# Performance work log

Measured on AMD Instinct MI355X. Metric: run time of the kernel, lower is better.

The kernel has to match this reference:

```python
import jax, jax.numpy as jnp
import numpy as np

K_FRAC = 0.5
NUM_CLASSES = 16
N = 8192
IN_DIM = 512
PER_CLASS = N // NUM_CLASSES          # 512 items per class (equal counts -> static shapes)
KK = int(K_FRAC * PER_CLASS)          # 256 kept per class


def setup_inputs() -> dict:
    key = jax.random.key(0)
    k1, k2, k3, k4 = jax.random.split(key, 4)
    M = jax.random.normal(k1, (1, N, N), dtype=jnp.float32)
    X = jax.random.normal(k2, (1, N, IN_DIM), dtype=jnp.float32)
    # class ids with exactly PER_CLASS members per class, randomly permuted
    mask = jax.random.permutation(k3, jnp.arange(N, dtype=jnp.int64) % NUM_CLASSES)[None, :]
    W = jax.random.normal(k4, (1, IN_DIM), dtype=jnp.float32) * 0.02
    b = jnp.zeros((1,), dtype=jnp.float32)
    return {"M": M, "X": X, "mask": mask, "W": W, "b": b}


def reference(M, X, mask, W, b):
    # scores = sigmoid(Linear(X) / 100), squeezed to [N] (batch == 1)
    scores = jax.nn.sigmoid((jnp.einsum('bnd,od->bno', X, W)[0, :, 0] + b[0]) / 100.0)  # [N]
    m0 = mask[-1]  # [N] class ids
    idx_parts, val_parts = [], []
    for j in range(NUM_CLASSES):  # fixed small loop over classes
        idx_j = jnp.nonzero(m0 == j, size=PER_CLASS, fill_value=0)[0]   # [PER_CLASS]
        way_scores = scores[idx_j]
        # top-k smallest of (way_scores - mean) == top-k largest of (mean - way_scores)
        _, way_idx = jax.lax.top_k(jnp.mean(way_scores) - way_scores, KK)
        val_parts.append(way_scores[way_idx])
        idx_parts.append(idx_j[way_idx])
    values = jnp.concatenate(val_parts)          # [NUM_CLASSES*KK]
    idx = jnp.concatenate(idx_parts)             # [NUM_CLASSES*KK]
    X_out = X[:, idx, :] * values[None, :, None] # gather + scale
    M_out = M[:, idx, :][:, :, idx]              # double gather (rows then cols)
    return (M_out, X_out, mask[:, idx])
```

## Files before the change

### kernel.cpp

```cpp
#include <hip/hip_runtime.h>

#define NN 8192
#define IN_DIM 512
#define NUM_CLASSES 16
#define PER_CLASS 512
#define KK 256
#define NSEL (NUM_CLASSES * KK)

typedef float vfloat4 __attribute__((ext_vector_type(4)));

__global__ __launch_bounds__(256) void scores_kernel(
    const float* __restrict__ X, const float* __restrict__ W,
    const float* __restrict__ b, float* __restrict__ scores) {
  const int wave = threadIdx.x >> 6;
  const int lane = threadIdx.x & 63;
  const int row  = blockIdx.x * (blockDim.x >> 6) + wave;
  if (row >= NN) return;

  const float4* xp = (const float4*)(X + (size_t)row * IN_DIM);
  const float4* wp = (const float4*)W;
  float acc = 0.f;
#pragma unroll
  for (int k = 0; k < 2; ++k) {
    const int i = lane + k * 64;
    const float4 xv = xp[i];
    const float4 wv = wp[i];
    acc += xv.x * wv.x + xv.y * wv.y + xv.z * wv.z + xv.w * wv.w;
  }
#pragma unroll
  for (int off = 32; off > 0; off >>= 1)
    acc += __shfl_xor(acc, off, 64);

  if (lane == 0) {
    const float z = (acc + b[0]) * 0.01f;
    scores[row] = 1.0f / (1.0f + expf(-z));
  }
}

__global__ __launch_bounds__(512) void select_kernel(
    const int* __restrict__ mask, const float* __restrict__ scores,
    int* __restrict__ sel_idx, float* __restrict__ sel_val) {
  const int cls  = blockIdx.x;
  const int tid  = threadIdx.x;
  const int lane = tid & 63;
  const int wave = tid >> 6;

  __shared__ int   members[PER_CLASS];
  __shared__ float ssc[PER_CLASS];
  __shared__ int   wave_tot[8];
  __shared__ int   running;
  __shared__ double wsum[8];
  __shared__ float meanf;

  if (tid == 0) running = 0;
  __syncthreads();

  for (int chunk = 0; chunk < NN; chunk += 512) {
    const int i = chunk + tid;
    const bool flag = (mask[i] == cls);
    const unsigned long long bal = __ballot(flag);
    const int pre = __popcll(bal & ((1ull << lane) - 1ull));
    if (lane == 0) wave_tot[wave] = __popcll(bal);
    __syncthreads();
    int woff = 0;
    for (int w = 0; w < wave; ++w) woff += wave_tot[w];
    const int pos = running + woff + pre;
    if (flag) members[pos] = i;
    __syncthreads();
    if (tid == 0) {
      int tot = 0;
      for (int w = 0; w < 8; ++w) tot += wave_tot[w];
      running += tot;
    }
    __syncthreads();
  }

  ssc[tid] = scores[members[tid]];
  __syncthreads();
  double v = (double)ssc[tid];
#pragma unroll
  for (int off = 32; off > 0; off >>= 1)
    v += __shfl_xor(v, off, 64);
  if (lane == 0) wsum[wave] = v;
  __syncthreads();
  if (tid == 0) {
    double s = 0.0;
    for (int w = 0; w < 8; ++w) s += wsum[w];
    meanf = (float)(s / (double)PER_CLASS);
  }
  __syncthreads();

  const float m = meanf;
  const float mykey = m - ssc[tid];
  int rank = 0;
  for (int u = 0; u < PER_CLASS; ++u) {
    const float ku = m - ssc[u];
    rank += (ku > mykey) || (ku == mykey && u < tid);
  }
  if (rank < KK) {
    sel_val[cls * KK + rank] = ssc[tid];
    sel_idx[cls * KK + rank] = members[tid];
  }
}

__global__ __launch_bounds__(512) void gather_kernel(
    const float* __restrict__ M, const float* __restrict__ X,
    const int* __restrict__ sel_idx, const float* __restrict__ sel_val,
    float* __restrict__ m_out, float* __restrict__ x_out,
    float* __restrict__ mask_out) {
  __shared__ float row[NN];
  const int r   = blockIdx.x;
  const int src = sel_idx[r];

  const vfloat4* mp = (const vfloat4*)(M + (size_t)src * NN);
  vfloat4* rp = (vfloat4*)row;
#pragma unroll
  for (int k = 0; k < 4; ++k) {
    const int i = k * 512 + threadIdx.x;
    rp[i] = __builtin_nontemporal_load(&mp[i]);
  }

  if (threadIdx.x < 128) {
    const float v = sel_val[r];
    const vfloat4 x =
        ((const vfloat4*)(X + (size_t)src * IN_DIM))[threadIdx.x];
    const vfloat4 o = x * v;
    __builtin_nontemporal_store(
        o, (vfloat4*)(x_out + (size_t)r * IN_DIM) + threadIdx.x);
  }
  if (threadIdx.x == 0) mask_out[r] = (float)(r >> 8);

  __syncthreads();

  vfloat4* out = (vfloat4*)(m_out + (size_t)r * NSEL);
  const int4* idx4 = (const int4*)sel_idx;
#pragma unroll
  for (int k = 0; k < 2; ++k) {
    const int c4 = k * 512 + threadIdx.x;
    const int4 id = idx4[c4];
    vfloat4 o;
    o.x = row[id.x]; o.y = row[id.y]; o.z = row[id.z]; o.w = row[id.w];
    __builtin_nontemporal_store(o, &out[c4]);
  }
}

extern "C" void kernel_launch(void* const* d_in, const int* in_sizes, int n_in,
                              void* d_out, int out_size, void* d_ws, size_t ws_size,
                              hipStream_t stream) {
  const float* M    = (const float*)d_in[0];
  const float* X    = (const float*)d_in[1];
  const int*   mask = (const int*)  d_in[2];
  const float* W    = (const float*)d_in[3];
  const float* b    = (const float*)d_in[4];

  float* out = (float*)d_out;
  float* m_out    = out;
  float* x_out    = out + (size_t)NSEL * NSEL;
  float* mask_out = x_out + (size_t)NSEL * IN_DIM;

  float* scores  = (float*)d_ws;
  int*   sel_idx = (int*)((char*)d_ws + NN * sizeof(float));
  float* sel_val = (float*)((char*)d_ws + NN * sizeof(float)
                                        + NSEL * sizeof(int));

  scores_kernel<<<NN / 4, 256, 0, stream>>>(X, W, b, scores);

  select_kernel<<<NUM_CLASSES, 512, 0, stream>>>(mask, scores, sel_idx, sel_val);

  gather_kernel<<<NSEL, 512, 0, stream>>>(M, X, sel_idx, sel_val,
                                          m_out, x_out, mask_out);
}
```

Baseline: 387.3 us.

## Fuse score and class-compaction into one kernel and split ranking across blocks

Class-member compaction moves out of the serial 16-chunk loop in select_kernel into a single pass inside a fused prep kernel. There, each thread scans 16 mask entries and the block does a wave prefix scan, running alongside the score blocks. The rank computation is spread over 4 blocks per class, with each output index split across 4 threads reading float4 keys and combining via shuffles. The gather kernel also hoists its index loads ahead of the row load. The intent is to shorten the small serial select stage that sits ahead of the bandwidth-bound gather, at the cost of recomputing the class mean in every block and extra workspace for the members array.

```diff
diff --git a/kernel.cpp b/kernel.cpp
--- a/kernel.cpp
+++ b/kernel.cpp
@@ -9,75 +9,88 @@
 
 typedef float vfloat4 __attribute__((ext_vector_type(4)));
 
-__global__ __launch_bounds__(256) void scores_kernel(
+__global__ __launch_bounds__(512) void prep_kernel(
     const float* __restrict__ X, const float* __restrict__ W,
-    const float* __restrict__ b, float* __restrict__ scores) {
-  const int wave = threadIdx.x >> 6;
-  const int lane = threadIdx.x & 63;
-  const int row  = blockIdx.x * (blockDim.x >> 6) + wave;
-  if (row >= NN) return;
-
-  const float4* xp = (const float4*)(X + (size_t)row * IN_DIM);
-  const float4* wp = (const float4*)W;
-  float acc = 0.f;
-#pragma unroll
-  for (int k = 0; k < 2; ++k) {
-    const int i = lane + k * 64;
-    const float4 xv = xp[i];
-    const float4 wv = wp[i];
-    acc += xv.x * wv.x + xv.y * wv.y + xv.z * wv.z + xv.w * wv.w;
-  }
-#pragma unroll
-  for (int off = 32; off > 0; off >>= 1)
-    acc += __shfl_xor(acc, off, 64);
-
-  if (lane == 0) {
-    const float z = (acc + b[0]) * 0.01f;
-    scores[row] = 1.0f / (1.0f + expf(-z));
-  }
-}
-
-__global__ __launch_bounds__(512) void select_kernel(
-    const int* __restrict__ mask, const float* __restrict__ scores,
-    int* __restrict__ sel_idx, float* __restrict__ sel_val) {
-  const int cls  = blockIdx.x;
+    const float* __restrict__ b, const int* __restrict__ mask,
+    float* __restrict__ scores, int* __restrict__ members) {
   const int tid  = threadIdx.x;
   const int lane = tid & 63;
   const int wave = tid >> 6;
 
-  __shared__ int   members[PER_CLASS];
-  __shared__ float ssc[PER_CLASS];
-  __shared__ int   wave_tot[8];
-  __shared__ int   running;
+  if (blockIdx.x < NUM_CLASSES) {
+    const int cls = blockIdx.x;
+    __shared__ int wave_tot[8];
+    const int base_i = tid * 16;
+    const int4* mp = (const int4*)(mask + base_i);
+    int flags = 0;
+#pragma unroll
+    for (int k = 0; k < 4; ++k) {
+      const int4 mv = mp[k];
+      flags |= (mv.x == cls) << (k * 4 + 0);
+      flags |= (mv.y == cls) << (k * 4 + 1);
+      flags |= (mv.z == cls) << (k * 4 + 2);
+      flags |= (mv.w == cls) << (k * 4 + 3);
+    }
+    const int cnt = __popc(flags);
+    int scan = cnt;
+#pragma unroll
+    for (int off = 1; off < 64; off <<= 1) {
+      const int n = __shfl_up(scan, off, 64);
+      if (lane >= off) scan += n;
+    }
+    if (lane == 63) wave_tot[wave] = scan;
+    __syncthreads();
+    int wbase = 0;
+    for (int w = 0; w < wave; ++w) wbase += wave_tot[w];
+    int pos = wbase + scan - cnt;
+    int* out = members + cls * PER_CLASS;
+    int f = flags;
+    while (f) {
+      const int k = __ffs(f) - 1;
+      f &= f - 1;
+      out[pos++] = base_i + k;
+    }
+  } else {
+    const int row = (blockIdx.x - NUM_CLASSES) * 8 + wave;
+    const float4* xp = (const float4*)(X + (size_t)row * IN_DIM);
+    const float4* wp = (const float4*)W;
+    float acc = 0.f;
+#pragma unroll
+    for (int k = 0; k < 2; ++k) {
+      const int i = lane + k * 64;
+      const float4 xv = xp[i];
+      const float4 wv = wp[i];
+      acc += xv.x * wv.x + xv.y * wv.y + xv.z * wv.z + xv.w * wv.w;
+    }
+#pragma unroll
+    for (int off = 32; off > 0; off >>= 1)
+      acc += __shfl_xor(acc, off, 64);
+    if (lane == 0) {
+      const float z = (acc + b[0]) * 0.01f;
+      scores[row] = 1.0f / (1.0f + expf(-z));
+    }
+  }
+}
+
+__global__ __launch_bounds__(512) void select_kernel(
+    const int* __restrict__ members, const float* __restrict__ scores,
+    int* __restrict__ sel_idx, float* __restrict__ sel_val) {
+  const int cls  = blockIdx.x >> 2;
+  const int q    = blockIdx.x & 3;
+  const int tid  = threadIdx.x;
+  const int lane = tid & 63;
+  const int wave = tid >> 6;
+
+  __shared__ float  ssc[PER_CLASS];
+  __shared__ float  keys[PER_CLASS];
   __shared__ double wsum[8];
-  __shared__ float meanf;
-
-  if (tid == 0) running = 0;
-  __syncthreads();
-
-  for (int chunk = 0; chunk < NN; chunk += 512) {
-    const int i = chunk + tid;
-    const bool flag = (mask[i] == cls);
-    const unsigned long long bal = __ballot(flag);
-    const int pre = __popcll(bal & ((1ull << lane) - 1ull));
-    if (lane == 0) wave_tot[wave] = __popcll(bal);
-    __syncthreads();
-    int woff = 0;
-    for (int w = 0; w < wave; ++w) woff += wave_tot[w];
-    const int pos = running + woff + pre;
-    if (flag) members[pos] = i;
-    __syncthreads();
-    if (tid == 0) {
-      int tot = 0;
-      for (int w = 0; w < 8; ++w) tot += wave_tot[w];
-      running += tot;
-    }
-    __syncthreads();
-  }
-
-  ssc[tid] = scores[members[tid]];
-  __syncthreads();
-  double v = (double)ssc[tid];
+  __shared__ float  meanf;
+
+  const int   mem_t = members[cls * PER_CLASS + tid];
+  const float sc_t  = scores[mem_t];
+  ssc[tid] = sc_t;
+
+  double v = (double)sc_t;
 #pragma unroll
   for (int off = 32; off > 0; off >>= 1)
     v += __shfl_xor(v, off, 64);
@@ -89,17 +102,30 @@
     meanf = (float)(s / (double)PER_CLASS);
   }
   __syncthreads();
-
   const float m = meanf;
-  const float mykey = m - ssc[tid];
+  keys[tid] = m - ssc[tid];
+  __syncthreads();
+
+  const int   j     = q * 128 + (tid >> 2);
+  const int   seg   = tid & 3;
+  const float mykey = keys[j];
   int rank = 0;
-  for (int u = 0; u < PER_CLASS; ++u) {
-    const float ku = m - ssc[u];
-    rank += (ku > mykey) || (ku == mykey && u < tid);
-  }
-  if (rank < KK) {
-    sel_val[cls * KK + rank] = ssc[tid];
-    sel_idx[cls * KK + rank] = members[tid];
+  const float4* k4  = (const float4*)(keys + seg * 128);
+  const int ubase   = seg * 128;
+#pragma unroll 4
+  for (int u4 = 0; u4 < 32; ++u4) {
+    const float4 kv = k4[u4];
+    const int u = ubase + u4 * 4;
+    rank += (kv.x > mykey) || (kv.x == mykey && (u + 0) < j);
+    rank += (kv.y > mykey) || (kv.y == mykey && (u + 1) < j);
+    rank += (kv.z > mykey) || (kv.z == mykey && (u + 2) < j);
+    rank += (kv.w > mykey) || (kv.w == mykey && (u + 3) < j);
+  }
+  rank += __shfl_xor(rank, 1, 64);
+  rank += __shfl_xor(rank, 2, 64);
+  if (seg == 0 && rank < KK) {
+    sel_val[cls * KK + rank] = ssc[j];
+    sel_idx[cls * KK + rank] = members[cls * PER_CLASS + j];
   }
 }
 
@@ -112,6 +138,10 @@
   const int r   = blockIdx.x;
   const int src = sel_idx[r];
 
+  const int4* idx4 = (const int4*)sel_idx;
+  const int4 id0 = idx4[threadIdx.x];
+  const int4 id1 = idx4[512 + threadIdx.x];
+
   const vfloat4* mp = (const vfloat4*)(M + (size_t)src * NN);
   vfloat4* rp = (vfloat4*)row;
 #pragma unroll
@@ -133,14 +163,15 @@
   __syncthreads();
 
   vfloat4* out = (vfloat4*)(m_out + (size_t)r * NSEL);
-  const int4* idx4 = (const int4*)sel_idx;
-#pragma unroll
-  for (int k = 0; k < 2; ++k) {
-    const int c4 = k * 512 + threadIdx.x;
-    const int4 id = idx4[c4];
+  {
     vfloat4 o;
-    o.x = row[id.x]; o.y = row[id.y]; o.z = row[id.z]; o.w = row[id.w];
-    __builtin_nontemporal_store(o, &out[c4]);
+    o.x = row[id0.x]; o.y = row[id0.y]; o.z = row[id0.z]; o.w = row[id0.w];
+    __builtin_nontemporal_store(o, &out[threadIdx.x]);
+  }
+  {
+    vfloat4 o;
+    o.x = row[id1.x]; o.y = row[id1.y]; o.z = row[id1.z]; o.w = row[id1.w];
+    __builtin_nontemporal_store(o, &out[512 + threadIdx.x]);
   }
 }
 
@@ -162,10 +193,15 @@
   int*   sel_idx = (int*)((char*)d_ws + NN * sizeof(float));
   float* sel_val = (float*)((char*)d_ws + NN * sizeof(float)
                                         + NSEL * sizeof(int));
-
-  scores_kernel<<<NN / 4, 256, 0, stream>>>(X, W, b, scores);
-
-  select_kernel<<<NUM_CLASSES, 512, 0, stream>>>(mask, scores, sel_idx, sel_val);
+  int*   members = (int*)((char*)d_ws + NN * sizeof(float)
+                                      + NSEL * sizeof(int)
+                                      + NSEL * sizeof(float));
+
+  prep_kernel<<<NUM_CLASSES + NN / 8, 512, 0, stream>>>(X, W, b, mask,
+                                                        scores, members);
+
+  select_kernel<<<NUM_CLASSES * 4, 512, 0, stream>>>(members, scores,
+                                                     sel_idx, sel_val);
 
   gather_kernel<<<NSEL, 512, 0, stream>>>(M, X, sel_idx, sel_val,
                                           m_out, x_out, mask_out);
```

Measured after the change: 361.4 us. 1.07x faster.
